# Kernel tuning notes

Hardware: AMD Instinct MI355X
Metric: run time of the kernel (lower is better)

The kernel has to match this reference:

```python
import jax, jax.numpy as jnp
import numpy as np

N_NODES = 100000
N_EDGES = 3200000
F_IN = 128
F_OUT = 128


def setup_inputs() -> dict:
    key = jax.random.key(0)
    k1, k2, k3 = jax.random.split(key, 3)
    x = jax.random.normal(k1, (N_NODES, F_IN), dtype=jnp.float32)
    edge_index = jax.random.randint(k2, (2, N_EDGES), 0, N_NODES, dtype=jnp.int64)
    # xavier_uniform for weight, zeros for bias
    limit = float(np.sqrt(6.0 / (F_IN + F_OUT)))
    weight = jax.random.uniform(k3, (F_IN, F_OUT), dtype=jnp.float32,
                                minval=-limit, maxval=limit)
    bias = jnp.zeros((F_OUT,), dtype=jnp.float32)
    return {"x": x, "edge_index": edge_index, "weight": weight, "bias": bias}


def reference(x, edge_index, weight, bias):
    num_nodes = x.shape[0]
    # add self loops
    loops = jnp.arange(num_nodes, dtype=edge_index.dtype)
    row = jnp.concatenate([edge_index[0], loops])  # [E+N]
    col = jnp.concatenate([edge_index[1], loops])  # [E+N]
    # degree from row (matches torch.bincount(row))
    deg = jnp.zeros((num_nodes,), dtype=x.dtype).at[row].add(1.0)
    deg_inv_sqrt = jnp.where(deg > 0, jax.lax.rsqrt(jnp.maximum(deg, 1.0)), 0.0)
    norm = deg_inv_sqrt[row] * deg_inv_sqrt[col]  # [E+N]
    # dense transform then sparse aggregation (gather-scale-scatter)
    support = x @ weight  # [N, F_OUT]
    msgs = support[col] * norm[:, None]  # [E+N, F_OUT]
    out = jax.ops.segment_sum(msgs, row, num_segments=num_nodes)
    return out + bias
```

## Files before the change

### kernel.cpp

```cpp
#include <hip/hip_runtime.h>
#include <hip/hip_fp16.h>

#define FDIM 128
#define SCAN_B 1024
#define NBUK 8
#define NCHK 32
#define MAXB 12544

typedef _Float16 half8 __attribute__((ext_vector_type(8)));
typedef float f32x4 __attribute__((ext_vector_type(4)));

__global__ void __launch_bounds__(1024) k_cnt(const int* __restrict__ row,
                                              int* __restrict__ cntC,
                                              int nE, int n, int bspan) {
    __shared__ int hist[MAXB];
    int bucket = blockIdx.x & (NBUK - 1);
    int chunk  = blockIdx.x >> 3;
    int lo  = bucket * bspan;
    int len = min(bspan, n - lo);
    for (int j = threadIdx.x; j < len; j += 1024) hist[j] = 0;
    __syncthreads();

    int per = (((nE + NCHK - 1) / NCHK) + 3) & ~3;
    int beg = chunk * per;
    int end = min(beg + per, nE);
    if (beg < end) {
        int nv = (end - beg) >> 2;
        const int4* row4 = reinterpret_cast<const int4*>(row + beg);
        for (int q = threadIdx.x; q < nv; q += 1024) {
            int4 r = row4[q];
            unsigned a;
            a = (unsigned)(r.x - lo); if (a < (unsigned)len) atomicAdd(&hist[a], 1);
            a = (unsigned)(r.y - lo); if (a < (unsigned)len) atomicAdd(&hist[a], 1);
            a = (unsigned)(r.z - lo); if (a < (unsigned)len) atomicAdd(&hist[a], 1);
            a = (unsigned)(r.w - lo); if (a < (unsigned)len) atomicAdd(&hist[a], 1);
        }
        for (int e = beg + (nv << 2) + threadIdx.x; e < end; e += 1024) {
            unsigned a = (unsigned)(row[e] - lo);
            if (a < (unsigned)len) atomicAdd(&hist[a], 1);
        }
    }
    __syncthreads();
    int* dst = cntC + (size_t)chunk * n + lo;
    for (int j = threadIdx.x; j < len; j += 1024) dst[j] = hist[j];
}

__global__ void __launch_bounds__(1024) k_scan_reduce(const int* __restrict__ cntC,
                                                      int* __restrict__ part, int n) {
    __shared__ int sd[1024];
    int i = blockIdx.x * SCAN_B + threadIdx.x;
    int v = 0;
    if (i < n) {
        v = 1;
        #pragma unroll
        for (int c = 0; c < NCHK; ++c) v += cntC[(size_t)c * n + i];
    }
    sd[threadIdx.x] = v;
    __syncthreads();
    for (int off = 512; off > 0; off >>= 1) {
        if (threadIdx.x < off) sd[threadIdx.x] += sd[threadIdx.x + off];
        __syncthreads();
    }
    if (threadIdx.x == 0) part[blockIdx.x] = sd[0];
}

__global__ void __launch_bounds__(128) k_scan_part(int* __restrict__ part,
                                                   int* __restrict__ offs,
                                                   int nb, int n) {
    __shared__ int sd[128];
    int v = (threadIdx.x < nb) ? part[threadIdx.x] : 0;
    sd[threadIdx.x] = v;
    __syncthreads();
    for (int off = 1; off < 128; off <<= 1) {
        int t = (threadIdx.x >= off) ? sd[threadIdx.x - off] : 0;
        __syncthreads();
        sd[threadIdx.x] += t;
        __syncthreads();
    }
    if (threadIdx.x < nb) part[threadIdx.x] = sd[threadIdx.x] - v;
    if (threadIdx.x == 127) offs[n] = sd[127];
}

__global__ void __launch_bounds__(1024) k_scan_final(int* __restrict__ cntC,
                                                     const int* __restrict__ part,
                                                     int* __restrict__ offs,
                                                     float* __restrict__ dis,
                                                     int* __restrict__ sc, int n) {
    __shared__ int sd[1024];
    int i = blockIdx.x * SCAN_B + threadIdx.x;
    int c[NCHK];
    int v = 0;
    if (i < n) {
        v = 1;
        #pragma unroll
        for (int x = 0; x < NCHK; ++x) { c[x] = cntC[(size_t)x * n + i]; v += c[x]; }
    }
    sd[threadIdx.x] = v;
    __syncthreads();
    for (int off = 1; off < 1024; off <<= 1) {
        int t = (threadIdx.x >= off) ? sd[threadIdx.x - off] : 0;
        __syncthreads();
        sd[threadIdx.x] += t;
        __syncthreads();
    }
    if (i < n) {
        int o = part[blockIdx.x] + sd[threadIdx.x] - v;
        offs[i] = o;
        dis[i]  = rsqrtf((float)v);
        sc[o]   = i;
        int b = o + 1;
        #pragma unroll
        for (int x = 0; x < NCHK; ++x) { cntC[(size_t)x * n + i] = b; b += c[x]; }
    }
}

__global__ void __launch_bounds__(1024) k_fillb(const int* __restrict__ row,
                                                const int* __restrict__ col,
                                                const int* __restrict__ curC,
                                                int* __restrict__ sc,
                                                int nE, int n, int bspan) {
    __shared__ int cur[MAXB];
    int bucket = blockIdx.x & (NBUK - 1);
    int chunk  = blockIdx.x >> 3;
    int lo  = bucket * bspan;
    int len = min(bspan, n - lo);
    const int* src = curC + (size_t)chunk * n + lo;
    for (int j = threadIdx.x; j < len; j += 1024) cur[j] = src[j];
    __syncthreads();

    int per = (((nE + NCHK - 1) / NCHK) + 3) & ~3;
    int beg = chunk * per;
    int end = min(beg + per, nE);
    if (beg < end) {
        int nv = (end - beg) >> 2;
        const int4* row4 = reinterpret_cast<const int4*>(row + beg);
        const int4* col4 = reinterpret_cast<const int4*>(col + beg);
        for (int q = threadIdx.x; q < nv; q += 1024) {
            int4 r  = row4[q];
            int4 cc = col4[q];
            unsigned a;
            a = (unsigned)(r.x - lo); if (a < (unsigned)len) sc[atomicAdd(&cur[a], 1)] = cc.x;
            a = (unsigned)(r.y - lo); if (a < (unsigned)len) sc[atomicAdd(&cur[a], 1)] = cc.y;
            a = (unsigned)(r.z - lo); if (a < (unsigned)len) sc[atomicAdd(&cur[a], 1)] = cc.z;
            a = (unsigned)(r.w - lo); if (a < (unsigned)len) sc[atomicAdd(&cur[a], 1)] = cc.w;
        }
        for (int e = beg + (nv << 2) + threadIdx.x; e < end; e += 1024) {
            unsigned a = (unsigned)(row[e] - lo);
            if (a < (unsigned)len) sc[atomicAdd(&cur[a], 1)] = col[e];
        }
    }
}

__global__ void __launch_bounds__(64) k_wprep(const float* __restrict__ w,
                                              half8* __restrict__ wfrag) {
    int fid = blockIdx.x;
    int nt = fid >> 2, ks = fid & 3;
    int lane = threadIdx.x;
    int c = lane & 15, kg = lane >> 4;
    int f  = nt * 16 + c;
    int k0 = ks * 32 + kg * 8;
    half8 hi, lo;
    #pragma unroll
    for (int j = 0; j < 8; ++j) {
        float v = w[(size_t)(k0 + j) * FDIM + f];
        _Float16 h = (_Float16)v;
        hi[j] = h;
        lo[j] = (_Float16)(v - (float)h);
    }
    wfrag[fid * 64 + lane]        = hi;
    wfrag[(32 + fid) * 64 + lane] = lo;
}

__global__ void __launch_bounds__(256) k_gemm(const float* __restrict__ x,
                                              const half8* __restrict__ wfrag,
                                              const float* __restrict__ dis,
                                              __half* __restrict__ support, int n) {
    int wave = threadIdx.x >> 6;
    int lane = threadIdx.x & 63;
    int wbase = blockIdx.x * 64 + wave * 16;
    int r  = lane & 15;
    int kg = lane >> 4;

    int noder = min(wbase + r, n - 1);
    const float* xp = x + (size_t)noder * FDIM + kg * 8;
    half8 ah[4], al[4];
    #pragma unroll
    for (int ks = 0; ks < 4; ++ks) {
        const float4* p = reinterpret_cast<const float4*>(xp + ks * 32);
        float4 f0 = p[0], f1 = p[1];
        float v[8] = {f0.x, f0.y, f0.z, f0.w, f1.x, f1.y, f1.z, f1.w};
        #pragma unroll
        for (int j = 0; j < 8; ++j) {
            _Float16 h = (_Float16)v[j];
            ah[ks][j] = h;
            al[ks][j] = (_Float16)(v[j] - (float)h);
        }
    }

    float d[4];
    #pragma unroll
    for (int i = 0; i < 4; ++i)
        d[i] = dis[min(wbase + kg * 4 + i, n - 1)];

    #pragma unroll
    for (int nt = 0; nt < 8; ++nt) {
        const half8* bp = wfrag + (size_t)(nt * 4) * 64 + lane;
        f32x4 acc = {0.f, 0.f, 0.f, 0.f};
        #pragma unroll
        for (int ks = 0; ks < 4; ++ks) {
            half8 bh = bp[ks * 64];
            half8 bl = bp[32 * 64 + ks * 64];
            acc = __builtin_amdgcn_mfma_f32_16x16x32_f16(ah[ks], bh, acc, 0, 0, 0);
            acc = __builtin_amdgcn_mfma_f32_16x16x32_f16(al[ks], bh, acc, 0, 0, 0);
            acc = __builtin_amdgcn_mfma_f32_16x16x32_f16(ah[ks], bl, acc, 0, 0, 0);
        }
        #pragma unroll
        for (int i = 0; i < 4; ++i) {
            int node = wbase + kg * 4 + i;
            if (node < n)
                support[(size_t)node * FDIM + nt * 16 + r] =
                    __float2half(d[i] * acc[i]);
        }
    }
}

__global__ void __launch_bounds__(64) k_agg(const __half2* __restrict__ sup2,
                                            const int* __restrict__ offs,
                                            const int* __restrict__ sc,
                                            const float* __restrict__ dis,
                                            const float* __restrict__ bias,
                                            float* __restrict__ out, int n) {
    int i  = blockIdx.x;
    int f2 = threadIdx.x;
    int beg = offs[i], end = offs[i + 1];
    float ax = 0.f, ay = 0.f;
    int j = beg;
    for (; j + 8 <= end; j += 8) {
        int c0 = sc[j],     c1 = sc[j + 1], c2 = sc[j + 2], c3 = sc[j + 3];
        int c4 = sc[j + 4], c5 = sc[j + 5], c6 = sc[j + 6], c7 = sc[j + 7];
        float2 v0 = __half22float2(sup2[(size_t)c0 * 64 + f2]);
        float2 v1 = __half22float2(sup2[(size_t)c1 * 64 + f2]);
        float2 v2 = __half22float2(sup2[(size_t)c2 * 64 + f2]);
        float2 v3 = __half22float2(sup2[(size_t)c3 * 64 + f2]);
        float2 v4 = __half22float2(sup2[(size_t)c4 * 64 + f2]);
        float2 v5 = __half22float2(sup2[(size_t)c5 * 64 + f2]);
        float2 v6 = __half22float2(sup2[(size_t)c6 * 64 + f2]);
        float2 v7 = __half22float2(sup2[(size_t)c7 * 64 + f2]);
        ax += ((v0.x + v1.x) + (v2.x + v3.x)) + ((v4.x + v5.x) + (v6.x + v7.x));
        ay += ((v0.y + v1.y) + (v2.y + v3.y)) + ((v4.y + v5.y) + (v6.y + v7.y));
    }
    for (; j + 4 <= end; j += 4) {
        int c0 = sc[j], c1 = sc[j + 1], c2 = sc[j + 2], c3 = sc[j + 3];
        float2 v0 = __half22float2(sup2[(size_t)c0 * 64 + f2]);
        float2 v1 = __half22float2(sup2[(size_t)c1 * 64 + f2]);
        float2 v2 = __half22float2(sup2[(size_t)c2 * 64 + f2]);
        float2 v3 = __half22float2(sup2[(size_t)c3 * 64 + f2]);
        ax += (v0.x + v1.x) + (v2.x + v3.x);
        ay += (v0.y + v1.y) + (v2.y + v3.y);
    }
    for (; j < end; ++j) {
        float2 v = __half22float2(sup2[(size_t)sc[j] * 64 + f2]);
        ax += v.x; ay += v.y;
    }
    float di = dis[i];
    const float2* b2 = reinterpret_cast<const float2*>(bias);
    float2 bb = b2[f2];
    float2 o;
    o.x = di * ax + bb.x;
    o.y = di * ay + bb.y;
    reinterpret_cast<float2*>(out)[(size_t)i * 64 + f2] = o;
}

extern "C" void kernel_launch(void* const* d_in, const int* in_sizes, int n_in,
                              void* d_out, int out_size, void* d_ws, size_t ws_size,
                              hipStream_t stream) {
    const float* x    = (const float*)d_in[0];
    const int*   ei   = (const int*)d_in[1];
    const float* w    = (const float*)d_in[2];
    const float* bias = (const float*)d_in[3];
    float*       out  = (float*)d_out;

    int n  = in_sizes[0] / FDIM;
    int nE = in_sizes[1] / 2;
    const int* row = ei;
    const int* col = ei + nE;
    int nbscan = (n + SCAN_B - 1) / SCAN_B;
    int bspan  = (n + NBUK - 1) / NBUK;

    char* ws = (char*)d_ws;
    size_t off = 0;
    auto alloc = [&](size_t bytes) -> void* {
        void* p = ws + off;
        off += (bytes + 255) & ~(size_t)255;
        return p;
    };
    __half* support = (__half*)alloc((size_t)n * FDIM * sizeof(__half));
    int*    cntC    = (int*)alloc((size_t)NCHK * n * sizeof(int));
    int*    offs    = (int*)alloc((size_t)(n + 1) * sizeof(int));
    int*    part    = (int*)alloc((size_t)128 * sizeof(int));
    float*  dis     = (float*)alloc((size_t)n * sizeof(float));
    int*    sc      = (int*)alloc((size_t)(nE + n) * sizeof(int));
    half8*  wfrag   = (half8*)alloc((size_t)64 * 64 * sizeof(half8));

    k_wprep      <<<32, 64, 0, stream>>>(w, wfrag);
    k_cnt        <<<NBUK * NCHK, 1024, 0, stream>>>(row, cntC, nE, n, bspan);
    k_scan_reduce<<<nbscan, 1024, 0, stream>>>(cntC, part, n);
    k_scan_part  <<<1, 128, 0, stream>>>(part, offs, nbscan, n);
    k_scan_final <<<nbscan, 1024, 0, stream>>>(cntC, part, offs, dis, sc, n);
    k_fillb      <<<NBUK * NCHK, 1024, 0, stream>>>(row, col, cntC, sc, nE, n, bspan);
    k_gemm       <<<(n + 63) / 64, 256, 0, stream>>>(x, wfrag, dis, support, n);
    k_agg        <<<n, 64, 0, stream>>>((const __half2*)support, offs,
                                        sc, dis, bias, out, n);
}
```

Measured before the change: 334.0 us.

## Fuse fill and GEMM into one launch, fold partial scan into final scan

```diff
diff --git a/kernel.cpp b/kernel.cpp
--- a/kernel.cpp
+++ b/kernel.cpp
@@ -6,6 +6,7 @@
 #define NBUK 8
 #define NCHK 32
 #define MAXB 12544
+#define NFB (NBUK * NCHK)
 
 typedef _Float16 half8 __attribute__((ext_vector_type(8)));
 typedef float f32x4 __attribute__((ext_vector_type(4)));
@@ -64,29 +65,29 @@
     if (threadIdx.x == 0) part[blockIdx.x] = sd[0];
 }
 
-__global__ void __launch_bounds__(128) k_scan_part(int* __restrict__ part,
-                                                   int* __restrict__ offs,
-                                                   int nb, int n) {
-    __shared__ int sd[128];
-    int v = (threadIdx.x < nb) ? part[threadIdx.x] : 0;
-    sd[threadIdx.x] = v;
-    __syncthreads();
-    for (int off = 1; off < 128; off <<= 1) {
-        int t = (threadIdx.x >= off) ? sd[threadIdx.x - off] : 0;
-        __syncthreads();
-        sd[threadIdx.x] += t;
-        __syncthreads();
-    }
-    if (threadIdx.x < nb) part[threadIdx.x] = sd[threadIdx.x] - v;
-    if (threadIdx.x == 127) offs[n] = sd[127];
-}
-
 __global__ void __launch_bounds__(1024) k_scan_final(int* __restrict__ cntC,
                                                      const int* __restrict__ part,
                                                      int* __restrict__ offs,
                                                      float* __restrict__ dis,
-                                                     int* __restrict__ sc, int n) {
+                                                     int* __restrict__ sc,
+                                                     int n, int nb) {
     __shared__ int sd[1024];
+    __shared__ int sdp[128];
+    int pv = 0;
+    if (threadIdx.x < 128) {
+        pv = (threadIdx.x < nb) ? part[threadIdx.x] : 0;
+        sdp[threadIdx.x] = pv;
+    }
+    __syncthreads();
+    for (int off = 1; off < 128; off <<= 1) {
+        int t = 0;
+        if (threadIdx.x < 128 && threadIdx.x >= off) t = sdp[threadIdx.x - off];
+        __syncthreads();
+        if (threadIdx.x < 128) sdp[threadIdx.x] += t;
+        __syncthreads();
+    }
+    int blockbase = (blockIdx.x == 0) ? 0 : sdp[blockIdx.x - 1];
+
     int i = blockIdx.x * SCAN_B + threadIdx.x;
     int c[NCHK];
     int v = 0;
@@ -104,8 +105,9 @@
         __syncthreads();
     }
     if (i < n) {
-        int o = part[blockIdx.x] + sd[threadIdx.x] - v;
+        int o = blockbase + sd[threadIdx.x] - v;
         offs[i] = o;
+        if (i == n - 1) offs[n] = o + v;
         dis[i]  = rsqrtf((float)v);
         sc[o]   = i;
         int b = o + 1;
@@ -114,112 +116,115 @@
     }
 }
 
-__global__ void __launch_bounds__(1024) k_fillb(const int* __restrict__ row,
-                                                const int* __restrict__ col,
-                                                const int* __restrict__ curC,
-                                                int* __restrict__ sc,
-                                                int nE, int n, int bspan) {
-    __shared__ int cur[MAXB];
-    int bucket = blockIdx.x & (NBUK - 1);
-    int chunk  = blockIdx.x >> 3;
-    int lo  = bucket * bspan;
-    int len = min(bspan, n - lo);
-    const int* src = curC + (size_t)chunk * n + lo;
-    for (int j = threadIdx.x; j < len; j += 1024) cur[j] = src[j];
-    __syncthreads();
-
-    int per = (((nE + NCHK - 1) / NCHK) + 3) & ~3;
-    int beg = chunk * per;
-    int end = min(beg + per, nE);
-    if (beg < end) {
-        int nv = (end - beg) >> 2;
-        const int4* row4 = reinterpret_cast<const int4*>(row + beg);
-        const int4* col4 = reinterpret_cast<const int4*>(col + beg);
-        for (int q = threadIdx.x; q < nv; q += 1024) {
-            int4 r  = row4[q];
-            int4 cc = col4[q];
-            unsigned a;
-            a = (unsigned)(r.x - lo); if (a < (unsigned)len) sc[atomicAdd(&cur[a], 1)] = cc.x;
-            a = (unsigned)(r.y - lo); if (a < (unsigned)len) sc[atomicAdd(&cur[a], 1)] = cc.y;
-            a = (unsigned)(r.z - lo); if (a < (unsigned)len) sc[atomicAdd(&cur[a], 1)] = cc.z;
-            a = (unsigned)(r.w - lo); if (a < (unsigned)len) sc[atomicAdd(&cur[a], 1)] = cc.w;
-        }
-        for (int e = beg + (nv << 2) + threadIdx.x; e < end; e += 1024) {
-            unsigned a = (unsigned)(row[e] - lo);
-            if (a < (unsigned)len) sc[atomicAdd(&cur[a], 1)] = col[e];
-        }
-    }
-}
-
-__global__ void __launch_bounds__(64) k_wprep(const float* __restrict__ w,
-                                              half8* __restrict__ wfrag) {
-    int fid = blockIdx.x;
-    int nt = fid >> 2, ks = fid & 3;
-    int lane = threadIdx.x;
-    int c = lane & 15, kg = lane >> 4;
-    int f  = nt * 16 + c;
-    int k0 = ks * 32 + kg * 8;
-    half8 hi, lo;
-    #pragma unroll
-    for (int j = 0; j < 8; ++j) {
-        float v = w[(size_t)(k0 + j) * FDIM + f];
-        _Float16 h = (_Float16)v;
-        hi[j] = h;
-        lo[j] = (_Float16)(v - (float)h);
-    }
-    wfrag[fid * 64 + lane]        = hi;
-    wfrag[(32 + fid) * 64 + lane] = lo;
-}
-
-__global__ void __launch_bounds__(256) k_gemm(const float* __restrict__ x,
-                                              const half8* __restrict__ wfrag,
-                                              const float* __restrict__ dis,
-                                              __half* __restrict__ support, int n) {
-    int wave = threadIdx.x >> 6;
-    int lane = threadIdx.x & 63;
-    int wbase = blockIdx.x * 64 + wave * 16;
-    int r  = lane & 15;
-    int kg = lane >> 4;
-
-    int noder = min(wbase + r, n - 1);
-    const float* xp = x + (size_t)noder * FDIM + kg * 8;
-    half8 ah[4], al[4];
-    #pragma unroll
-    for (int ks = 0; ks < 4; ++ks) {
-        const float4* p = reinterpret_cast<const float4*>(xp + ks * 32);
-        float4 f0 = p[0], f1 = p[1];
-        float v[8] = {f0.x, f0.y, f0.z, f0.w, f1.x, f1.y, f1.z, f1.w};
-        #pragma unroll
-        for (int j = 0; j < 8; ++j) {
-            _Float16 h = (_Float16)v[j];
-            ah[ks][j] = h;
-            al[ks][j] = (_Float16)(v[j] - (float)h);
-        }
-    }
-
-    float d[4];
-    #pragma unroll
-    for (int i = 0; i < 4; ++i)
-        d[i] = dis[min(wbase + kg * 4 + i, n - 1)];
-
-    #pragma unroll
-    for (int nt = 0; nt < 8; ++nt) {
-        const half8* bp = wfrag + (size_t)(nt * 4) * 64 + lane;
-        f32x4 acc = {0.f, 0.f, 0.f, 0.f};
+__global__ void __launch_bounds__(1024) k_fuse(const int* __restrict__ row,
+                                               const int* __restrict__ col,
+                                               int* __restrict__ curC,
+                                               int* __restrict__ sc,
+                                               const float* __restrict__ x,
+                                               const float* __restrict__ w,
+                                               const float* __restrict__ dis,
+                                               __half* __restrict__ support,
+                                               int nE, int n, int bspan) {
+    __shared__ char smraw[65536];
+
+    if (blockIdx.x < NFB) {
+        int* cur = reinterpret_cast<int*>(smraw);
+        int bucket = blockIdx.x & (NBUK - 1);
+        int chunk  = blockIdx.x >> 3;
+        int lo  = bucket * bspan;
+        int len = min(bspan, n - lo);
+        const int* src = curC + (size_t)chunk * n + lo;
+        for (int j = threadIdx.x; j < len; j += 1024) cur[j] = src[j];
+        __syncthreads();
+
+        int per = (((nE + NCHK - 1) / NCHK) + 3) & ~3;
+        int beg = chunk * per;
+        int end = min(beg + per, nE);
+        if (beg < end) {
+            int nv = (end - beg) >> 2;
+            const int4* row4 = reinterpret_cast<const int4*>(row + beg);
+            const int4* col4 = reinterpret_cast<const int4*>(col + beg);
+            for (int q = threadIdx.x; q < nv; q += 1024) {
+                int4 r  = row4[q];
+                int4 cc = col4[q];
+                unsigned a;
+                a = (unsigned)(r.x - lo); if (a < (unsigned)len) sc[atomicAdd(&cur[a], 1)] = cc.x;
+                a = (unsigned)(r.y - lo); if (a < (unsigned)len) sc[atomicAdd(&cur[a], 1)] = cc.y;
+                a = (unsigned)(r.z - lo); if (a < (unsigned)len) sc[atomicAdd(&cur[a], 1)] = cc.z;
+                a = (unsigned)(r.w - lo); if (a < (unsigned)len) sc[atomicAdd(&cur[a], 1)] = cc.w;
+            }
+            for (int e = beg + (nv << 2) + threadIdx.x; e < end; e += 1024) {
+                unsigned a = (unsigned)(row[e] - lo);
+                if (a < (unsigned)len) sc[atomicAdd(&cur[a], 1)] = col[e];
+            }
+        }
+    } else {
+        half8* smw = reinterpret_cast<half8*>(smraw);
+        for (int e = threadIdx.x; e < 2048; e += 1024) {
+            int fid = e >> 6, lane = e & 63;
+            int nt = fid >> 2, ks = fid & 3;
+            int f  = nt * 16 + (lane & 15);
+            int k0 = ks * 32 + (lane >> 4) * 8;
+            half8 hi, lo;
+            #pragma unroll
+            for (int j = 0; j < 8; ++j) {
+                float v = w[(size_t)(k0 + j) * FDIM + f];
+                _Float16 h = (_Float16)v;
+                hi[j] = h;
+                lo[j] = (_Float16)(v - (float)h);
+            }
+            smw[e]        = hi;
+            smw[2048 + e] = lo;
+        }
+        __syncthreads();
+
+        int wave = threadIdx.x >> 6;
+        int lane = threadIdx.x & 63;
+        int wbase = (blockIdx.x - NFB) * 256 + wave * 16;
+        if (wbase >= n) return;
+        int r  = lane & 15;
+        int kg = lane >> 4;
+
+        int noder = min(wbase + r, n - 1);
+        const float* xp = x + (size_t)noder * FDIM + kg * 8;
+        half8 ah[4], al[4];
         #pragma unroll
         for (int ks = 0; ks < 4; ++ks) {
-            half8 bh = bp[ks * 64];
-            half8 bl = bp[32 * 64 + ks * 64];
-            acc = __builtin_amdgcn_mfma_f32_16x16x32_f16(ah[ks], bh, acc, 0, 0, 0);
-            acc = __builtin_amdgcn_mfma_f32_16x16x32_f16(al[ks], bh, acc, 0, 0, 0);
-            acc = __builtin_amdgcn_mfma_f32_16x16x32_f16(ah[ks], bl, acc, 0, 0, 0);
-        }
-        #pragma unroll
-        for (int i = 0; i < 4; ++i) {
-            int node = wbase + kg * 4 + i;
-            if (node < n)
-                support[(size_t)node * FDIM + nt * 16 + r] =
-                    __float2half(d[i] * acc[i]);
+            const float4* p = reinterpret_cast<const float4*>(xp + ks * 32);
+            float4 f0 = p[0], f1 = p[1];
+            float v[8] = {f0.x, f0.y, f0.z, f0.w, f1.x, f1.y, f1.z, f1.w};
+            #pragma unroll
+            for (int j = 0; j < 8; ++j) {
+                _Float16 h = (_Float16)v[j];
+                ah[ks][j] = h;
+                al[ks][j] = (_Float16)(v[j] - (float)h);
+            }
+        }
+
+        float d[4];
+        #pragma unroll
+        for (int i = 0; i < 4; ++i)
+            d[i] = dis[min(wbase + kg * 4 + i, n - 1)];
+
+        #pragma unroll
+        for (int nt = 0; nt < 8; ++nt) {
+            const half8* bp = smw + (size_t)(nt * 4) * 64 + lane;
+            f32x4 acc = {0.f, 0.f, 0.f, 0.f};
+            #pragma unroll
+            for (int ks = 0; ks < 4; ++ks) {
+                half8 bh = bp[ks * 64];
+                half8 bl = bp[2048 + ks * 64];
+                acc = __builtin_amdgcn_mfma_f32_16x16x32_f16(ah[ks], bh, acc, 0, 0, 0);
+                acc = __builtin_amdgcn_mfma_f32_16x16x32_f16(al[ks], bh, acc, 0, 0, 0);
+                acc = __builtin_amdgcn_mfma_f32_16x16x32_f16(ah[ks], bl, acc, 0, 0, 0);
+            }
+            #pragma unroll
+            for (int i = 0; i < 4; ++i) {
+                int node = wbase + kg * 4 + i;
+                if (node < n)
+                    support[(size_t)node * FDIM + nt * 16 + r] =
+                        __float2half(d[i] * acc[i]);
+            }
         }
     }
 }
@@ -286,6 +291,7 @@
     const int* col = ei + nE;
     int nbscan = (n + SCAN_B - 1) / SCAN_B;
     int bspan  = (n + NBUK - 1) / NBUK;
+    int ngb    = (n + 255) / 256;
 
     char* ws = (char*)d_ws;
     size_t off = 0;
@@ -300,15 +306,12 @@
     int*    part    = (int*)alloc((size_t)128 * sizeof(int));
     float*  dis     = (float*)alloc((size_t)n * sizeof(float));
     int*    sc      = (int*)alloc((size_t)(nE + n) * sizeof(int));
-    half8*  wfrag   = (half8*)alloc((size_t)64 * 64 * sizeof(half8));
-
-    k_wprep      <<<32, 64, 0, stream>>>(w, wfrag);
+
     k_cnt        <<<NBUK * NCHK, 1024, 0, stream>>>(row, cntC, nE, n, bspan);
     k_scan_reduce<<<nbscan, 1024, 0, stream>>>(cntC, part, n);
-    k_scan_part  <<<1, 128, 0, stream>>>(part, offs, nbscan, n);
-    k_scan_final <<<nbscan, 1024, 0, stream>>>(cntC, part, offs, dis, sc, n);
-    k_fillb      <<<NBUK * NCHK, 1024, 0, stream>>>(row, col, cntC, sc, nE, n, bspan);
-    k_gemm       <<<(n + 63) / 64, 256, 0, stream>>>(x, wfrag, dis, support, n);
+    k_scan_final <<<nbscan, 1024, 0, stream>>>(cntC, part, offs, dis, sc, n, nbscan);
+    k_fuse       <<<NFB + ngb, 1024, 0, stream>>>(row, col, cntC, sc,
+                                                  x, w, dis, support, nE, n, bspan);
     k_agg        <<<n, 64, 0, stream>>>((const __half2*)support, offs,
                                         sc, dis, bias, out, n);
 }
```

Measured after the change: 322.2 us. -3.5%, faster.
